# Kernel optimization log

Hardware: AMD Instinct MI355X
Metric: run time of the kernel (lower is better)

The kernel has to match this reference:

```python
import jax, jax.numpy as jnp
import numpy as np

# --- gate hyperparameters (from init config) ---
DIM = 2048
N_EXPERTS = 256
TOPK = 8
N_GROUPS = 8
TOPK_GROUPS = 4
GROUP_TOPK = 2
ROUTE_SCALE = 2.5
T_TOKENS = 32768
NEG_INF = jnp.float32(-1e30)


def setup_inputs() -> dict:
    key = jax.random.key(0)
    kx, kw, kb = jax.random.split(key, 3)
    x = jax.random.normal(kx, (T_TOKENS, DIM), dtype=jnp.float32)
    # nn.init.normal_(weight, std=0.006)
    weight = 0.006 * jax.random.normal(kw, (N_EXPERTS, DIM), dtype=jnp.float32)
    # bias buffer starts at zero but gets adjusted; use small nonzero values so it matters
    bias = 0.001 * jax.random.normal(kb, (N_EXPERTS,), dtype=jnp.float32)
    return {"x": x, "weight": weight, "bias": bias}


def reference(x, weight, bias):
    T = x.shape[0]
    # scores = sigmoid(x @ W^T)  -> (T, E)
    scores = jax.nn.sigmoid(jnp.einsum("td,ed->te", x, weight))
    biased = scores + bias.astype(scores.dtype)  # (T, E)

    # --- group-limited routing ---
    epg = N_EXPERTS // N_GROUPS
    bg = biased.reshape(T, N_GROUPS, epg)  # (T, G, E/G)
    # group score = sum of top-`GROUP_TOPK` biased scores within each group
    group_scores = jax.lax.top_k(bg, GROUP_TOPK)[0].sum(axis=-1)  # (T, G)
    top_groups = jax.lax.top_k(group_scores, TOPK_GROUPS)[1]  # (T, topk_groups)
    keep = jnp.zeros((T, N_GROUPS), dtype=bool).at[
        jnp.arange(T)[:, None], top_groups
    ].set(True)  # (T, G)
    biased = jnp.where(keep[:, :, None], bg, NEG_INF).reshape(T, N_EXPERTS)

    # --- final top-k over biased scores; weights from RAW sigmoid scores ---
    indices = jax.lax.top_k(biased, TOPK)[1]  # (T, topk) int32
    weights = jnp.take_along_axis(scores, indices, axis=1)  # (T, topk)
    weights = weights / jnp.maximum(
        weights.sum(axis=-1, keepdims=True), jnp.float32(1e-10)
    )
    weights = (weights * jnp.float32(ROUTE_SCALE)).astype(x.dtype)
    return weights, indices
```

## Files before the change

### kernel.cpp

```cpp
#include <hip/hip_runtime.h>
#include <math.h>

#define T_TOKENS 32768
#define DIM 2048
#define N_EXPERTS 256
#define N_GROUPS 8
#define EPG 32
#define TOPK 8
#define TOPK_GROUPS 4
#define ROUTE_SCALE 2.5f

#define BM 64
#define BK 32
#define KITERS (DIM / BK)
#define W_SCALE 256.0f
#define INV_W_SCALE (1.0f / 256.0f)

#define A_OFF 0
#define BH_OFF 8192
#define BL_OFF 24576

typedef unsigned short u16;
typedef _Float16 f16x8 __attribute__((ext_vector_type(8)));
typedef float f32x4 __attribute__((ext_vector_type(4)));

__device__ __forceinline__ u16 f16_bits(_Float16 h) {
    union { _Float16 f; u16 u; } c; c.f = h; return c.u;
}

__device__ __forceinline__ void gload16(const void* g, void* l) {
    __builtin_amdgcn_global_load_lds(
        (const __attribute__((address_space(1))) void*)g,
        (__attribute__((address_space(3))) void*)l, 16, 0, 0);
}

__global__ __launch_bounds__(256) void convert_w(
    const float* __restrict__ W, u16* __restrict__ Whi, u16* __restrict__ Wlo)
{
    const int i = blockIdx.x * 256 + threadIdx.x;
    const float x = W[i] * W_SCALE;
    const _Float16 hi = (_Float16)x;
    const _Float16 lo = (_Float16)(x - (float)hi);
    Whi[i] = f16_bits(hi);
    Wlo[i] = f16_bits(lo);
}

__device__ __forceinline__ void split8(const float4 p, const float4 q,
                                       f16x8* hi, f16x8* lo)
{
    const float v[8] = {p.x, p.y, p.z, p.w, q.x, q.y, q.z, q.w};
    #pragma unroll
    for (int k = 0; k < 8; k++) {
        const _Float16 h = (_Float16)v[k];
        (*hi)[k] = h;
        (*lo)[k] = (_Float16)(v[k] - (float)h);
    }
}

__global__ __launch_bounds__(512, 4) void fused_gate(
    const float* __restrict__ X,
    const u16* __restrict__ Whi, const u16* __restrict__ Wlo,
    const float* __restrict__ bias,
    float* __restrict__ out_w, float* __restrict__ out_i)
{
    __shared__ __align__(16) char smem[65536];
    float* Sc = (float*)smem;

    const int tid = threadIdx.x;
    const int m0 = blockIdx.x * BM;
    const int lane = tid & 63;
    const int wave = tid >> 6;
    const int wm = wave >> 2;
    const int wn = wave & 3;
    const int l16 = lane & 15;
    const int quad = lane >> 4;

    char* const aDst   = smem + A_OFF  + wave * 1024;
    char* const bhDst0 = smem + BH_OFF + wave * 2048;
    char* const bhDst1 = bhDst0 + 1024;
    char* const blDst0 = smem + BL_OFF + wave * 2048;
    char* const blDst1 = blDst0 + 1024;

    const int aRow  = wave * 8 + (lane >> 3);
    const int aColb = ((lane & 7) ^ (lane >> 3)) << 4;
    const char* aSrc = (const char*)X + (size_t)(m0 + aRow) * (DIM * 4) + aColb;

    const int bRow0 = wave * 32 + (lane >> 2);
    const int bRow1 = bRow0 + 16;
    const int bColb = ((lane & 3) ^ ((lane >> 3) & 3)) << 4;
    const char* bhSrc0 = (const char*)Whi + (size_t)bRow0 * (DIM * 2) + bColb;
    const char* bhSrc1 = (const char*)Whi + (size_t)bRow1 * (DIM * 2) + bColb;
    const char* blSrc0 = (const char*)Wlo + (size_t)bRow0 * (DIM * 2) + bColb;
    const char* blSrc1 = (const char*)Wlo + (size_t)bRow1 * (DIM * 2) + bColb;

    int aP[2], bP[4];
    #pragma unroll
    for (int i = 0; i < 2; i++) {
        const int r = wm * 32 + i * 16 + l16;
        aP[i] = A_OFF + r * 128 + ((quad * 32) ^ ((r & 7) << 4));
    }
    #pragma unroll
    for (int j = 0; j < 4; j++) {
        const int r = wn * 64 + j * 16 + l16;
        bP[j] = r * 64 + ((quad * 16) ^ (((r >> 1) & 3) << 4));
    }

    f32x4 acc[2][4];
    #pragma unroll
    for (int i = 0; i < 2; i++)
        #pragma unroll
        for (int j = 0; j < 4; j++) acc[i][j] = (f32x4){0.f, 0.f, 0.f, 0.f};

    float4 ra[2][2];
    f16x8 fbh[4], fbl[4];

    gload16(aSrc, aDst);
    gload16(bhSrc0, bhDst0);
    gload16(bhSrc1, bhDst1);
    gload16(blSrc0, blDst0);
    gload16(blSrc1, blDst1);
    __syncthreads();
    #pragma unroll
    for (int i = 0; i < 2; i++) {
        ra[i][0] = *(const float4*)(smem + aP[i]);
        ra[i][1] = *(const float4*)(smem + (aP[i] ^ 16));
    }
    #pragma unroll
    for (int j = 0; j < 4; j++) {
        fbh[j] = *(const f16x8*)(smem + BH_OFF + bP[j]);
        fbl[j] = *(const f16x8*)(smem + BL_OFF + bP[j]);
    }

    #pragma unroll 1
    for (int it = 0; it < KITERS; ++it) {
        __syncthreads();
        if (it + 1 < KITERS) {
            const size_t ao = (size_t)(it + 1) * 128;
            const size_t bo = (size_t)(it + 1) * 64;
            gload16(aSrc + ao, aDst);
            gload16(bhSrc0 + bo, bhDst0);
            gload16(bhSrc1 + bo, bhDst1);
            gload16(blSrc0 + bo, blDst0);
            gload16(blSrc1 + bo, blDst1);
        }

        f16x8 fah[2], fal[2];
        split8(ra[0][0], ra[0][1], &fah[0], &fal[0]);
        split8(ra[1][0], ra[1][1], &fah[1], &fal[1]);
        #pragma unroll
        for (int i = 0; i < 2; i++)
            #pragma unroll
            for (int j = 0; j < 4; j++) {
                acc[i][j] = __builtin_amdgcn_mfma_f32_16x16x32_f16(fah[i], fbh[j], acc[i][j], 0, 0, 0);
                acc[i][j] = __builtin_amdgcn_mfma_f32_16x16x32_f16(fah[i], fbl[j], acc[i][j], 0, 0, 0);
                acc[i][j] = __builtin_amdgcn_mfma_f32_16x16x32_f16(fal[i], fbh[j], acc[i][j], 0, 0, 0);
            }

        __syncthreads();
        if (it + 1 < KITERS) {
            #pragma unroll
            for (int i = 0; i < 2; i++) {
                ra[i][0] = *(const float4*)(smem + aP[i]);
                ra[i][1] = *(const float4*)(smem + (aP[i] ^ 16));
            }
            #pragma unroll
            for (int j = 0; j < 4; j++) {
                fbh[j] = *(const f16x8*)(smem + BH_OFF + bP[j]);
                fbl[j] = *(const f16x8*)(smem + BL_OFF + bP[j]);
            }
        }
    }

    float bv[4];
    #pragma unroll
    for (int j = 0; j < 4; j++) bv[j] = bias[wn * 64 + j * 16 + l16];

    #pragma unroll
    for (int i = 0; i < 2; i++)
        #pragma unroll
        for (int j = 0; j < 4; j++)
            #pragma unroll
            for (int r = 0; r < 4; r++) {
                const int trow = wm * 32 + i * 16 + quad * 4 + r;
                const int e = wn * 64 + j * 16 + l16;
                const float logit = acc[i][j][r] * INV_W_SCALE;
                const float s = 1.f / (1.f + expf(-logit));
                Sc[trow * N_EXPERTS + e] = s + bv[j];
            }
    __syncthreads();

    if (tid < 64) {
        const float* row = Sc + tid * N_EXPERTS;

        float gs[N_GROUPS];
        #pragma unroll
        for (int g = 0; g < N_GROUPS; g++) {
            float m1 = -INFINITY, m2 = -INFINITY;
            #pragma unroll
            for (int jj = 0; jj < EPG; jj++) {
                const float v = row[g * EPG + ((tid + jj) & (EPG - 1))];
                if (v > m1) { m2 = m1; m1 = v; }
                else if (v > m2) { m2 = v; }
            }
            gs[g] = m1 + m2;
        }
        unsigned keep = 0;
        #pragma unroll
        for (int g = 0; g < N_GROUPS; g++) {
            int cnt = 0;
            #pragma unroll
            for (int h = 0; h < N_GROUPS; h++)
                if (gs[h] > gs[g] || (gs[h] == gs[g] && h < g)) cnt++;
            if (cnt < TOPK_GROUPS) keep |= (1u << g);
        }
        float tv[TOPK]; int ti[TOPK];
        #pragma unroll
        for (int i = 0; i < TOPK; i++) { tv[i] = -INFINITY; ti[i] = 0x7fffffff; }
        for (int g = 0; g < N_GROUPS; g++) {
            if (!(keep & (1u << g))) continue;
            #pragma unroll 4
            for (int jj = 0; jj < EPG; jj++) {
                const int e = g * EPG + ((tid + jj) & (EPG - 1));
                const float v = row[e];
                if (v > tv[TOPK - 1] || (v == tv[TOPK - 1] && e < ti[TOPK - 1])) {
                    float cv = v; int ce = e;
                    #pragma unroll
                    for (int s = 0; s < TOPK; s++) {
                        const bool b = (cv > tv[s]) || (cv == tv[s] && ce < ti[s]);
                        if (b) {
                            const float t1 = tv[s]; tv[s] = cv; cv = t1;
                            const int t2 = ti[s]; ti[s] = ce; ce = t2;
                        }
                    }
                }
            }
        }
        float w[TOPK], sum = 0.f;
        #pragma unroll
        for (int i = 0; i < TOPK; i++) {
            w[i] = row[ti[i]] - bias[ti[i]];
            sum += w[i];
        }
        const float scale = ROUTE_SCALE / fmaxf(sum, 1e-10f);
        const size_t t = (size_t)m0 + tid;
        #pragma unroll
        for (int i = 0; i < TOPK; i++) {
            out_w[t * TOPK + i] = w[i] * scale;
            out_i[t * TOPK + i] = (float)ti[i];
        }
    }
}

extern "C" void kernel_launch(void* const* d_in, const int* in_sizes, int n_in,
                              void* d_out, int out_size, void* d_ws, size_t ws_size,
                              hipStream_t stream)
{
    const float* x = (const float*)d_in[0];
    const float* w = (const float*)d_in[1];
    const float* b = (const float*)d_in[2];

    u16* whi = (u16*)d_ws;
    u16* wlo = whi + (size_t)N_EXPERTS * DIM;

    float* out_w = (float*)d_out;
    float* out_i = (float*)d_out + (size_t)T_TOKENS * TOPK;

    convert_w<<<(N_EXPERTS * DIM) / 256, 256, 0, stream>>>(w, whi, wlo);
    fused_gate<<<T_TOKENS / BM, 512, 0, stream>>>(x, whi, wlo, b, out_w, out_i);
}
```

Before: 551.8 us.

## Double-buffer LDS tiles in the gate GEMM, one barrier per K-step

Adds a second 40 KB shared-memory buffer so the next K-tile's global-to-LDS loads target the buffer not being read. The main loop is unrolled by two and alternates buffers, with one __syncthreads per K-step instead of two. The register prefetch of fragments from LDS is dropped: fragments are now read just before the MFMAs that use them. Shared memory grows from 64 KB to 80 KB per block, which may reduce how many blocks fit on a CU, and LDS read latency is no longer hidden by the register prefetch.

```diff
diff --git a/kernel.cpp b/kernel.cpp
--- a/kernel.cpp
+++ b/kernel.cpp
@@ -19,6 +19,7 @@
 #define A_OFF 0
 #define BH_OFF 8192
 #define BL_OFF 24576
+#define BUF_STRIDE 40960
 
 typedef unsigned short u16;
 typedef _Float16 f16x8 __attribute__((ext_vector_type(8)));
@@ -63,7 +64,7 @@
     const float* __restrict__ bias,
     float* __restrict__ out_w, float* __restrict__ out_i)
 {
-    __shared__ __align__(16) char smem[65536];
+    __shared__ __align__(16) char smem[81920];
     float* Sc = (float*)smem;
 
     const int tid = threadIdx.x;
@@ -111,53 +112,26 @@
         #pragma unroll
         for (int j = 0; j < 4; j++) acc[i][j] = (f32x4){0.f, 0.f, 0.f, 0.f};
 
-    float4 ra[2][2];
-    f16x8 fbh[4], fbl[4];
-
     gload16(aSrc, aDst);
     gload16(bhSrc0, bhDst0);
     gload16(bhSrc1, bhDst1);
     gload16(blSrc0, blDst0);
     gload16(blSrc1, blDst1);
     __syncthreads();
-    #pragma unroll
-    for (int i = 0; i < 2; i++) {
-        ra[i][0] = *(const float4*)(smem + aP[i]);
-        ra[i][1] = *(const float4*)(smem + (aP[i] ^ 16));
-    }
-    #pragma unroll
-    for (int j = 0; j < 4; j++) {
-        fbh[j] = *(const f16x8*)(smem + BH_OFF + bP[j]);
-        fbl[j] = *(const f16x8*)(smem + BL_OFF + bP[j]);
-    }
 
     #pragma unroll 1
-    for (int it = 0; it < KITERS; ++it) {
-        __syncthreads();
-        if (it + 1 < KITERS) {
+    for (int it = 0; it < KITERS; it += 2) {
+        {
             const size_t ao = (size_t)(it + 1) * 128;
             const size_t bo = (size_t)(it + 1) * 64;
-            gload16(aSrc + ao, aDst);
-            gload16(bhSrc0 + bo, bhDst0);
-            gload16(bhSrc1 + bo, bhDst1);
-            gload16(blSrc0 + bo, blDst0);
-            gload16(blSrc1 + bo, blDst1);
-        }
-
-        f16x8 fah[2], fal[2];
-        split8(ra[0][0], ra[0][1], &fah[0], &fal[0]);
-        split8(ra[1][0], ra[1][1], &fah[1], &fal[1]);
-        #pragma unroll
-        for (int i = 0; i < 2; i++)
-            #pragma unroll
-            for (int j = 0; j < 4; j++) {
-                acc[i][j] = __builtin_amdgcn_mfma_f32_16x16x32_f16(fah[i], fbh[j], acc[i][j], 0, 0, 0);
-                acc[i][j] = __builtin_amdgcn_mfma_f32_16x16x32_f16(fah[i], fbl[j], acc[i][j], 0, 0, 0);
-                acc[i][j] = __builtin_amdgcn_mfma_f32_16x16x32_f16(fal[i], fbh[j], acc[i][j], 0, 0, 0);
-            }
-
-        __syncthreads();
-        if (it + 1 < KITERS) {
+            gload16(aSrc + ao, aDst + BUF_STRIDE);
+            gload16(bhSrc0 + bo, bhDst0 + BUF_STRIDE);
+            gload16(bhSrc1 + bo, bhDst1 + BUF_STRIDE);
+            gload16(blSrc0 + bo, blDst0 + BUF_STRIDE);
+            gload16(blSrc1 + bo, blDst1 + BUF_STRIDE);
+
+            float4 ra[2][2];
+            f16x8 fbh[4], fbl[4], fah[2], fal[2];
             #pragma unroll
             for (int i = 0; i < 2; i++) {
                 ra[i][0] = *(const float4*)(smem + aP[i]);
@@ -168,6 +142,51 @@
                 fbh[j] = *(const f16x8*)(smem + BH_OFF + bP[j]);
                 fbl[j] = *(const f16x8*)(smem + BL_OFF + bP[j]);
             }
+            split8(ra[0][0], ra[0][1], &fah[0], &fal[0]);
+            split8(ra[1][0], ra[1][1], &fah[1], &fal[1]);
+            #pragma unroll
+            for (int i = 0; i < 2; i++)
+                #pragma unroll
+                for (int j = 0; j < 4; j++) {
+                    acc[i][j] = __builtin_amdgcn_mfma_f32_16x16x32_f16(fah[i], fbh[j], acc[i][j], 0, 0, 0);
+                    acc[i][j] = __builtin_amdgcn_mfma_f32_16x16x32_f16(fah[i], fbl[j], acc[i][j], 0, 0, 0);
+                    acc[i][j] = __builtin_amdgcn_mfma_f32_16x16x32_f16(fal[i], fbh[j], acc[i][j], 0, 0, 0);
+                }
+            __syncthreads();
+        }
+        {
+            if (it + 2 < KITERS) {
+                const size_t ao = (size_t)(it + 2) * 128;
+                const size_t bo = (size_t)(it + 2) * 64;
+                gload16(aSrc + ao, aDst);
+                gload16(bhSrc0 + bo, bhDst0);
+                gload16(bhSrc1 + bo, bhDst1);
+                gload16(blSrc0 + bo, blDst0);
+                gload16(blSrc1 + bo, blDst1);
+            }
+            float4 ra[2][2];
+            f16x8 fbh[4], fbl[4], fah[2], fal[2];
+            #pragma unroll
+            for (int i = 0; i < 2; i++) {
+                ra[i][0] = *(const float4*)(smem + BUF_STRIDE + aP[i]);
+                ra[i][1] = *(const float4*)(smem + BUF_STRIDE + (aP[i] ^ 16));
+            }
+            #pragma unroll
+            for (int j = 0; j < 4; j++) {
+                fbh[j] = *(const f16x8*)(smem + BUF_STRIDE + BH_OFF + bP[j]);
+                fbl[j] = *(const f16x8*)(smem + BUF_STRIDE + BL_OFF + bP[j]);
+            }
+            split8(ra[0][0], ra[0][1], &fah[0], &fal[0]);
+            split8(ra[1][0], ra[1][1], &fah[1], &fal[1]);
+            #pragma unroll
+            for (int i = 0; i < 2; i++)
+                #pragma unroll
+                for (int j = 0; j < 4; j++) {
+                    acc[i][j] = __builtin_amdgcn_mfma_f32_16x16x32_f16(fah[i], fbh[j], acc[i][j], 0, 0, 0);
+                    acc[i][j] = __builtin_amdgcn_mfma_f32_16x16x32_f16(fah[i], fbl[j], acc[i][j], 0, 0, 0);
+                    acc[i][j] = __builtin_amdgcn_mfma_f32_16x16x32_f16(fal[i], fbh[j], acc[i][j], 0, 0, 0);
+                }
+            __syncthreads();
         }
     }
 
```

After: 542.7 us. No clear change (-1.6%).
